# Performance work log

Hardware: AMD Instinct MI355X
Metric: run time of the kernel (lower is better)

## Reference

```python
import jax, jax.numpy as jnp
import numpy as np

# CrossAttention (DFFNet): 1x1 convs produce q,k from depth and v from rgb;
# full dense attention over hw spatial tokens: softmax(q^T k) then v @ mask^T.

def setup_inputs() -> dict:
    key = jax.random.key(0)
    ks = jax.random.split(key, 8)
    B, C, H, W = 4, 256, 64, 64
    Cqk = C // 8  # ratio=8 -> 32
    s = 0.02
    return {
        "rgb":   jax.random.normal(ks[0], (B, C, H, W), jnp.float32),
        "depth": jax.random.normal(ks[1], (B, C, H, W), jnp.float32),
        "Wq": jax.random.normal(ks[2], (Cqk, C), jnp.float32) * s,
        "bq": jax.random.normal(ks[3], (Cqk,), jnp.float32) * s,
        "Wk": jax.random.normal(ks[4], (Cqk, C), jnp.float32) * s,
        "bk": jax.random.normal(ks[5], (Cqk,), jnp.float32) * s,
        "Wv": jax.random.normal(ks[6], (C, C), jnp.float32) * s,
        "bv": jax.random.normal(ks[7], (C,), jnp.float32) * s,
    }


def reference(rgb, depth, Wq, bq, Wk, bk, Wv, bv):
    B, C, H, W = rgb.shape
    hw = H * W
    d = depth.reshape(B, C, hw)   # [B, C, hw]
    r = rgb.reshape(B, C, hw)     # [B, C, hw]
    # 1x1 convs == channel-mixing linear maps
    q = jnp.einsum('oc,bcn->bon', Wq, d) + bq[None, :, None]  # [B, Cqk, hw]
    k = jnp.einsum('oc,bcn->bon', Wk, d) + bk[None, :, None]  # [B, Cqk, hw]
    v = jnp.einsum('oc,bcn->bon', Wv, r) + bv[None, :, None]  # [B, C, hw]
    # scores: q^T k -> [B, hw, hw], softmax over last dim
    scores = jnp.einsum('bcn,bcm->bnm', q, k)
    mask = jax.nn.softmax(scores, axis=-1)
    # feat = v @ mask^T  -> [B, C, hw]
    feat = jnp.einsum('bcm,bnm->bcn', v, mask)
    return feat.reshape(B, C, H, W)
```

## Files before the change

kernel.cpp:

```cpp
#include <hip/hip_runtime.h>
#include <stdint.h>

#define L2E 1.44269504088896340736f

typedef _Float16 half8 __attribute__((ext_vector_type(8)));
typedef float floatx4 __attribute__((ext_vector_type(4)));

static __device__ __forceinline__ unsigned short f32_to_f16u(float f) {
  union { _Float16 h; unsigned short s; } cv; cv.h = (_Float16)f; return cv.s;
}

typedef __attribute__((address_space(3))) unsigned int as3_uint;
typedef __attribute__((address_space(1))) const unsigned int as1_cuint;

static __device__ __forceinline__ void async16(const void* g, void* l) {
  __builtin_amdgcn_global_load_lds((as1_cuint*)g, (as3_uint*)l, 16, 0, 0);
}

__global__ __launch_bounds__(256) void proj_kernel(
    const float* __restrict__ rgb,
    const float* __restrict__ depth,
    const float* __restrict__ Wq, const float* __restrict__ bq,
    const float* __restrict__ Wk, const float* __restrict__ bk,
    const float* __restrict__ Wv, const float* __restrict__ bv,
    unsigned short* __restrict__ qT,
    unsigned short* __restrict__ kT,
    unsigned short* __restrict__ v)
{
  __shared__ __align__(16) unsigned short sW[64 * 256];

  const int n0 = blockIdx.x * 64;
  const int b  = blockIdx.y;
  const int z  = blockIdx.z;
  const int t  = threadIdx.x;
  const int w  = t >> 6;
  const int lane = t & 63;
  const int l15 = lane & 15;
  const int q4  = lane >> 4;

  const float* X = (z == 0) ? depth : rgb;
  const float* xb = X + (size_t)b * 256 * 4096;
  const int n_row = n0 + 16 * w + l15;
  const int colbase = (z == 0) ? 0 : (z - 1) * 64;

#pragma unroll
  for (int it = 0; it < 8; it++) {
    int L = it * 256 + t;
    int og = L >> 5;
    int phys = L & 31;
    int ci = phys ^ (og & 7);
    const float* wr;
    if (z == 0) wr = (og < 32) ? (Wq + (size_t)og * 256) : (Wk + (size_t)(og - 32) * 256);
    else        wr = Wv + (size_t)(colbase + og) * 256;
    float4 w0 = *(const float4*)(wr + ci * 8);
    float4 w1 = *(const float4*)(wr + ci * 8 + 4);
    half8 h;
    h[0] = (_Float16)w0.x; h[1] = (_Float16)w0.y; h[2] = (_Float16)w0.z; h[3] = (_Float16)w0.w;
    h[4] = (_Float16)w1.x; h[5] = (_Float16)w1.y; h[6] = (_Float16)w1.z; h[7] = (_Float16)w1.w;
    *(half8*)&sW[(size_t)L * 8] = h;
  }

  float bias[4];
#pragma unroll
  for (int ct = 0; ct < 4; ct++) {
    int og = ct * 16 + l15;
    if (z == 0) bias[ct] = (og < 32) ? bq[og] : bk[og - 32];
    else        bias[ct] = bv[colbase + og];
  }
  __syncthreads();

  floatx4 acc[4];
#pragma unroll
  for (int i = 0; i < 4; i++) acc[i] = (floatx4){0.f, 0.f, 0.f, 0.f};

#pragma unroll
  for (int ks = 0; ks < 8; ks++) {
    const int c0 = ks * 32;
    half8 a;
#pragma unroll
    for (int j = 0; j < 8; j++) {
      int c = c0 + q4 * 8 + j;
      a[j] = (_Float16)xb[(size_t)c * 4096 + n_row];
    }
    const int ci = ks * 4 + q4;
#pragma unroll
    for (int ct = 0; ct < 4; ct++) {
      int og = ct * 16 + l15;
      half8 bf = *(const half8*)&sW[og * 256 + ((ci ^ (og & 7)) * 8)];
      acc[ct] = __builtin_amdgcn_mfma_f32_16x16x32_f16(a, bf, acc[ct], 0, 0, 0);
    }
  }

  __syncthreads();

  if (z == 0) {
#pragma unroll
    for (int ct = 0; ct < 4; ct++) {
      int og = ct * 16 + l15;
#pragma unroll
      for (int r = 0; r < 4; r++) {
        int n = n0 + 16 * w + q4 * 4 + r;
        unsigned short hv = f32_to_f16u(acc[ct][r] + bias[ct]);
        if (og < 32) qT[((size_t)b * 4096 + n) * 32 + og] = hv;
        else         kT[((size_t)b * 4096 + n) * 32 + (og - 32)] = hv;
      }
    }
  } else {
    unsigned short* tile = sW;
#pragma unroll
    for (int ct = 0; ct < 4; ct++) {
#pragma unroll
      for (int r = 0; r < 4; r++) {
        int co_l = ct * 16 + l15;
        int nl = 16 * w + q4 * 4 + r;
        tile[co_l * 72 + nl] = f32_to_f16u(acc[ct][r] + bias[ct]);
      }
    }
    __syncthreads();
#pragma unroll
    for (int it = 0; it < 2; it++) {
      int co_l = it * 32 + (t >> 3);
      int ch = t & 7;
      int4 val = *(const int4*)&tile[co_l * 72 + ch * 8];
      *(int4*)&v[((size_t)b * 256 + colbase + co_l) * 4096 + n0 + ch * 8] = val;
    }
  }
}

static __device__ __forceinline__ void stage_v(
    const unsigned short* __restrict__ vB, unsigned char* sbase,
    int m0, int t, int w)
{
#pragma unroll
  for (int j = 0; j < 4; j++) {
    int lin = j * 256 + t;
    int c = lin >> 2;
    int p = lin & 3;
    int lc = p ^ ((c >> 1) & 3);
    async16(&vB[(size_t)c * 4096 + m0 + lc * 8], sbase + j * 4096 + w * 1024);
  }
}

__global__ __launch_bounds__(256, 4) void attn_kernel(
    const unsigned short* __restrict__ qT,
    const unsigned short* __restrict__ kT,
    const unsigned short* __restrict__ v,
    unsigned short* __restrict__ Op,
    float* __restrict__ lW)
{
  __shared__ __align__(16) unsigned char smem[37888];
  unsigned short* sP = (unsigned short*)(smem + 32768);

  const int n0 = blockIdx.x * 64;
  const int b  = blockIdx.y;
  const int chunk = blockIdx.z;
  const int t  = threadIdx.x;
  const int w  = t >> 6;
  const int lane = t & 63;
  const int l15 = lane & 15;
  const int q4  = lane >> 4;

  half8 aq = *(const half8*)(qT + ((size_t)b * 4096 + n0 + 16 * w + l15) * 32 + q4 * 8);

  const unsigned short* vB = v + (size_t)b * 256 * 4096;
  const unsigned short* kL = kT + (size_t)b * 4096 * 32 + (size_t)l15 * 32 + q4 * 8;
  unsigned short* sPw = sP + w * 640;

  float lsum[4] = {0.f, 0.f, 0.f, 0.f};
  floatx4 acc[16];
#pragma unroll
  for (int ct = 0; ct < 16; ct++) acc[ct] = (floatx4){0.f, 0.f, 0.f, 0.f};
  const floatx4 zf = (floatx4){0.f, 0.f, 0.f, 0.f};

  const int mbase = chunk * 1024;

  stage_v(vB, smem, mbase, t, w);
  half8 kc0 = *(const half8*)(kL + (size_t)mbase * 32);
  half8 kc1 = *(const half8*)(kL + (size_t)(mbase + 16) * 32);

  int bufoff = 0;
  for (int it = 0; it < 32; ++it) {
    const int m0 = mbase + it * 32;
    half8 kn0 = kc0, kn1 = kc1;
    if (it < 31) {
      stage_v(vB, smem + (bufoff ^ 16384), m0 + 32, t, w);
      kn0 = *(const half8*)(kL + (size_t)(m0 + 32) * 32);
      kn1 = *(const half8*)(kL + (size_t)(m0 + 48) * 32);
      asm volatile("s_waitcnt vmcnt(6)" ::: "memory");
    } else {
      asm volatile("s_waitcnt vmcnt(0)" ::: "memory");
    }

    floatx4 s0 = __builtin_amdgcn_mfma_f32_16x16x32_f16(aq, kc0, zf, 0, 0, 0);
    floatx4 s1 = __builtin_amdgcn_mfma_f32_16x16x32_f16(aq, kc1, zf, 0, 0, 0);

    float p0[4], p1[4];
#pragma unroll
    for (int r = 0; r < 4; r++) {
      p0[r] = exp2f(s0[r] * L2E);
      p1[r] = exp2f(s1[r] * L2E);
      lsum[r] += p0[r] + p1[r];
    }
#pragma unroll
    for (int r = 0; r < 4; r++) {
      int row = q4 * 4 + r;
      sPw[row * 40 + l15]      = f32_to_f16u(p0[r]);
      sPw[row * 40 + 16 + l15] = f32_to_f16u(p1[r]);
    }
    asm volatile("s_waitcnt lgkmcnt(0)" ::: "memory");
    half8 ap = *(const half8*)&sPw[l15 * 40 + q4 * 8];

    __builtin_amdgcn_s_barrier();
    asm volatile("s_waitcnt lgkmcnt(0)" ::: "memory");

    const unsigned short* sVb = (const unsigned short*)(smem + bufoff);
#pragma unroll
    for (int ct = 0; ct < 16; ct++) {
      int co = ct * 16 + l15;
      half8 bv8 = *(const half8*)&sVb[co * 32 + ((q4 ^ ((co >> 1) & 3)) * 8)];
      acc[ct] = __builtin_amdgcn_mfma_f32_16x16x32_f16(ap, bv8, acc[ct], 0, 0, 0);
    }
    asm volatile("s_waitcnt lgkmcnt(0)" ::: "memory");
    __builtin_amdgcn_s_barrier();

    kc0 = kn0; kc1 = kn1;
    bufoff ^= 16384;
  }

#pragma unroll
  for (int off = 1; off < 16; off <<= 1) {
#pragma unroll
    for (int r = 0; r < 4; r++) lsum[r] += __shfl_xor(lsum[r], off);
  }
  if (l15 == 0) {
#pragma unroll
    for (int r = 0; r < 4; r++)
      lW[((size_t)chunk * 4 + b) * 4096 + n0 + 16 * w + q4 * 4 + r] = lsum[r];
  }

  unsigned short* sO = (unsigned short*)smem;
#pragma unroll
  for (int pass = 0; pass < 2; pass++) {
    __syncthreads();
#pragma unroll
    for (int cl = 0; cl < 8; cl++) {
      int ct = pass * 8 + cl;
      int co_l = cl * 16 + l15;
#pragma unroll
      for (int r = 0; r < 4; r++) {
        int nl = 16 * w + q4 * 4 + r;
        sO[co_l * 72 + nl] = f32_to_f16u(acc[ct][r]);
      }
    }
    __syncthreads();
#pragma unroll
    for (int s = 0; s < 4; s++) {
      int co_l = s * 32 + (t >> 3);
      int ch = t & 7;
      int4 val = *(const int4*)&sO[co_l * 72 + ch * 8];
      *(int4*)&Op[(((size_t)chunk * 4 + b) * 256 + pass * 128 + co_l) * 4096 + n0 + ch * 8] = val;
    }
  }
}

__global__ __launch_bounds__(256) void combine_kernel(
    const unsigned short* __restrict__ Op,
    const float* __restrict__ lW,
    float* __restrict__ out)
{
  const int t = threadIdx.x;
  const int b = blockIdx.y;
  const size_t n8 = (size_t)blockIdx.x * 2048 + (size_t)t * 8;
  const int co0 = blockIdx.z * 8;

  float sum[8] = {0.f, 0.f, 0.f, 0.f, 0.f, 0.f, 0.f, 0.f};
#pragma unroll
  for (int ch = 0; ch < 4; ch++) {
    const float* lp = lW + ((size_t)ch * 4 + b) * 4096 + n8;
    float4 a0 = *(const float4*)lp;
    float4 a1 = *(const float4*)(lp + 4);
    sum[0] += a0.x; sum[1] += a0.y; sum[2] += a0.z; sum[3] += a0.w;
    sum[4] += a1.x; sum[5] += a1.y; sum[6] += a1.z; sum[7] += a1.w;
  }
  float rl[8];
#pragma unroll
  for (int i = 0; i < 8; i++) rl[i] = 1.0f / sum[i];

#pragma unroll
  for (int cc = 0; cc < 8; cc++) {
    int co = co0 + cc;
    float o[8] = {0.f, 0.f, 0.f, 0.f, 0.f, 0.f, 0.f, 0.f};
#pragma unroll
    for (int ch = 0; ch < 4; ch++) {
      half8 hv = *(const half8*)&Op[(((size_t)ch * 4 + b) * 256 + co) * 4096 + n8];
#pragma unroll
      for (int i = 0; i < 8; i++) o[i] += (float)hv[i];
    }
    float* op = out + ((size_t)b * 256 + co) * 4096 + n8;
    float4 r0, r1;
    r0.x = o[0] * rl[0]; r0.y = o[1] * rl[1]; r0.z = o[2] * rl[2]; r0.w = o[3] * rl[3];
    r1.x = o[4] * rl[4]; r1.y = o[5] * rl[5]; r1.z = o[6] * rl[6]; r1.w = o[7] * rl[7];
    *(float4*)op = r0;
    *(float4*)(op + 4) = r1;
  }
}

extern "C" void kernel_launch(void* const* d_in, const int* in_sizes, int n_in,
                              void* d_out, int out_size, void* d_ws, size_t ws_size,
                              hipStream_t stream) {
  const float* rgb   = (const float*)d_in[0];
  const float* depth = (const float*)d_in[1];
  const float* Wq    = (const float*)d_in[2];
  const float* bq    = (const float*)d_in[3];
  const float* Wk    = (const float*)d_in[4];
  const float* bk    = (const float*)d_in[5];
  const float* Wv    = (const float*)d_in[6];
  const float* bv    = (const float*)d_in[7];
  float* out = (float*)d_out;

  unsigned short* qT = (unsigned short*)d_ws;
  unsigned short* kT = qT + (size_t)4 * 4096 * 32;
  unsigned short* vW = kT + (size_t)4 * 4096 * 32;
  unsigned short* Op = vW + (size_t)4 * 256 * 4096;
  float* lW = (float*)(Op + (size_t)4 * 4 * 256 * 4096);

  dim3 pg(64, 4, 5);
  proj_kernel<<<pg, 256, 0, stream>>>(rgb, depth, Wq, bq, Wk, bk, Wv, bv, qT, kT, vW);
  dim3 ag(64, 4, 4);
  attn_kernel<<<ag, 256, 0, stream>>>(qT, kT, vW, Op, lW);
  dim3 cg(2, 4, 32);
  combine_kernel<<<cg, 256, 0, stream>>>(Op, lW, out);
}
```

Measured before the change: 168.1 us.

## Reuse loaded activations across V channel groups and retile attention PV per wave

The projection kernel now loads each thread's input activation fragment into registers once and loops over two 64-channel output groups of V per block. This halves the grid's z extent and avoids re-reading the rgb tensor for each group. In the attention kernel, each wave now owns a 64-channel slice of V and reads all four waves' P tiles from shared memory. Each V fragment is then reused across four MFMAs instead of every wave loading all 256 V channels, which cuts LDS read traffic but needs the whole shared P buffer visible after the barrier.

```diff
diff --git a/kernel.cpp b/kernel.cpp
--- a/kernel.cpp
+++ b/kernel.cpp
@@ -41,88 +41,96 @@
   const float* X = (z == 0) ? depth : rgb;
   const float* xb = X + (size_t)b * 256 * 4096;
   const int n_row = n0 + 16 * w + l15;
-  const int colbase = (z == 0) ? 0 : (z - 1) * 64;
-
-#pragma unroll
-  for (int it = 0; it < 8; it++) {
-    int L = it * 256 + t;
-    int og = L >> 5;
-    int phys = L & 31;
-    int ci = phys ^ (og & 7);
-    const float* wr;
-    if (z == 0) wr = (og < 32) ? (Wq + (size_t)og * 256) : (Wk + (size_t)(og - 32) * 256);
-    else        wr = Wv + (size_t)(colbase + og) * 256;
-    float4 w0 = *(const float4*)(wr + ci * 8);
-    float4 w1 = *(const float4*)(wr + ci * 8 + 4);
-    half8 h;
-    h[0] = (_Float16)w0.x; h[1] = (_Float16)w0.y; h[2] = (_Float16)w0.z; h[3] = (_Float16)w0.w;
-    h[4] = (_Float16)w1.x; h[5] = (_Float16)w1.y; h[6] = (_Float16)w1.z; h[7] = (_Float16)w1.w;
-    *(half8*)&sW[(size_t)L * 8] = h;
-  }
-
-  float bias[4];
-#pragma unroll
-  for (int ct = 0; ct < 4; ct++) {
-    int og = ct * 16 + l15;
-    if (z == 0) bias[ct] = (og < 32) ? bq[og] : bk[og - 32];
-    else        bias[ct] = bv[colbase + og];
-  }
-  __syncthreads();
-
-  floatx4 acc[4];
-#pragma unroll
-  for (int i = 0; i < 4; i++) acc[i] = (floatx4){0.f, 0.f, 0.f, 0.f};
-
+
+  half8 a8[8];
 #pragma unroll
   for (int ks = 0; ks < 8; ks++) {
-    const int c0 = ks * 32;
-    half8 a;
 #pragma unroll
     for (int j = 0; j < 8; j++) {
-      int c = c0 + q4 * 8 + j;
-      a[j] = (_Float16)xb[(size_t)c * 4096 + n_row];
-    }
-    const int ci = ks * 4 + q4;
+      int c = ks * 32 + q4 * 8 + j;
+      a8[ks][j] = (_Float16)xb[(size_t)c * 4096 + n_row];
+    }
+  }
+
+  const int nq = (z == 0) ? 1 : 2;
+  for (int qd = 0; qd < nq; qd++) {
+    const int colbase = (z == 0) ? 0 : (z - 1) * 128 + qd * 64;
+    __syncthreads();
+
+#pragma unroll
+    for (int it = 0; it < 8; it++) {
+      int L = it * 256 + t;
+      int og = L >> 5;
+      int phys = L & 31;
+      int ci = phys ^ (og & 7);
+      const float* wr;
+      if (z == 0) wr = (og < 32) ? (Wq + (size_t)og * 256) : (Wk + (size_t)(og - 32) * 256);
+      else        wr = Wv + (size_t)(colbase + og) * 256;
+      float4 w0 = *(const float4*)(wr + ci * 8);
+      float4 w1 = *(const float4*)(wr + ci * 8 + 4);
+      half8 h;
+      h[0] = (_Float16)w0.x; h[1] = (_Float16)w0.y; h[2] = (_Float16)w0.z; h[3] = (_Float16)w0.w;
+      h[4] = (_Float16)w1.x; h[5] = (_Float16)w1.y; h[6] = (_Float16)w1.z; h[7] = (_Float16)w1.w;
+      *(half8*)&sW[(size_t)L * 8] = h;
+    }
+
+    float bias[4];
 #pragma unroll
     for (int ct = 0; ct < 4; ct++) {
       int og = ct * 16 + l15;
-      half8 bf = *(const half8*)&sW[og * 256 + ((ci ^ (og & 7)) * 8)];
-      acc[ct] = __builtin_amdgcn_mfma_f32_16x16x32_f16(a, bf, acc[ct], 0, 0, 0);
-    }
-  }
-
-  __syncthreads();
-
-  if (z == 0) {
-#pragma unroll
-    for (int ct = 0; ct < 4; ct++) {
-      int og = ct * 16 + l15;
-#pragma unroll
-      for (int r = 0; r < 4; r++) {
-        int n = n0 + 16 * w + q4 * 4 + r;
-        unsigned short hv = f32_to_f16u(acc[ct][r] + bias[ct]);
-        if (og < 32) qT[((size_t)b * 4096 + n) * 32 + og] = hv;
-        else         kT[((size_t)b * 4096 + n) * 32 + (og - 32)] = hv;
-      }
-    }
-  } else {
-    unsigned short* tile = sW;
-#pragma unroll
-    for (int ct = 0; ct < 4; ct++) {
-#pragma unroll
-      for (int r = 0; r < 4; r++) {
-        int co_l = ct * 16 + l15;
-        int nl = 16 * w + q4 * 4 + r;
-        tile[co_l * 72 + nl] = f32_to_f16u(acc[ct][r] + bias[ct]);
-      }
-    }
-    __syncthreads();
-#pragma unroll
-    for (int it = 0; it < 2; it++) {
-      int co_l = it * 32 + (t >> 3);
-      int ch = t & 7;
-      int4 val = *(const int4*)&tile[co_l * 72 + ch * 8];
-      *(int4*)&v[((size_t)b * 256 + colbase + co_l) * 4096 + n0 + ch * 8] = val;
+      if (z == 0) bias[ct] = (og < 32) ? bq[og] : bk[og - 32];
+      else        bias[ct] = bv[colbase + og];
+    }
+    __syncthreads();
+
+    floatx4 acc[4];
+#pragma unroll
+    for (int i = 0; i < 4; i++) acc[i] = (floatx4){0.f, 0.f, 0.f, 0.f};
+
+#pragma unroll
+    for (int ks = 0; ks < 8; ks++) {
+      const int ci = ks * 4 + q4;
+#pragma unroll
+      for (int ct = 0; ct < 4; ct++) {
+        int og = ct * 16 + l15;
+        half8 bf = *(const half8*)&sW[og * 256 + ((ci ^ (og & 7)) * 8)];
+        acc[ct] = __builtin_amdgcn_mfma_f32_16x16x32_f16(a8[ks], bf, acc[ct], 0, 0, 0);
+      }
+    }
+
+    __syncthreads();
+
+    if (z == 0) {
+#pragma unroll
+      for (int ct = 0; ct < 4; ct++) {
+        int og = ct * 16 + l15;
+#pragma unroll
+        for (int r = 0; r < 4; r++) {
+          int n = n0 + 16 * w + q4 * 4 + r;
+          unsigned short hv = f32_to_f16u(acc[ct][r] + bias[ct]);
+          if (og < 32) qT[((size_t)b * 4096 + n) * 32 + og] = hv;
+          else         kT[((size_t)b * 4096 + n) * 32 + (og - 32)] = hv;
+        }
+      }
+    } else {
+      unsigned short* tile = sW;
+#pragma unroll
+      for (int ct = 0; ct < 4; ct++) {
+#pragma unroll
+        for (int r = 0; r < 4; r++) {
+          int co_l = ct * 16 + l15;
+          int nl = 16 * w + q4 * 4 + r;
+          tile[co_l * 72 + nl] = f32_to_f16u(acc[ct][r] + bias[ct]);
+        }
+      }
+      __syncthreads();
+#pragma unroll
+      for (int it = 0; it < 2; it++) {
+        int co_l = it * 32 + (t >> 3);
+        int ch = t & 7;
+        int4 val = *(const int4*)&tile[co_l * 72 + ch * 8];
+        *(int4*)&v[((size_t)b * 256 + colbase + co_l) * 4096 + n0 + ch * 8] = val;
+      }
     }
   }
 }
@@ -208,17 +216,23 @@
       sPw[row * 40 + 16 + l15] = f32_to_f16u(p1[r]);
     }
     asm volatile("s_waitcnt lgkmcnt(0)" ::: "memory");
-    half8 ap = *(const half8*)&sPw[l15 * 40 + q4 * 8];
 
     __builtin_amdgcn_s_barrier();
     asm volatile("s_waitcnt lgkmcnt(0)" ::: "memory");
 
+    half8 ap[4];
+#pragma unroll
+    for (int nt = 0; nt < 4; nt++)
+      ap[nt] = *(const half8*)&sP[nt * 640 + l15 * 40 + q4 * 8];
+
     const unsigned short* sVb = (const unsigned short*)(smem + bufoff);
 #pragma unroll
-    for (int ct = 0; ct < 16; ct++) {
-      int co = ct * 16 + l15;
+    for (int ct = 0; ct < 4; ct++) {
+      int co = w * 64 + ct * 16 + l15;
       half8 bv8 = *(const half8*)&sVb[co * 32 + ((q4 ^ ((co >> 1) & 3)) * 8)];
-      acc[ct] = __builtin_amdgcn_mfma_f32_16x16x32_f16(ap, bv8, acc[ct], 0, 0, 0);
+#pragma unroll
+      for (int nt = 0; nt < 4; nt++)
+        acc[ct * 4 + nt] = __builtin_amdgcn_mfma_f32_16x16x32_f16(ap[nt], bv8, acc[ct * 4 + nt], 0, 0, 0);
     }
     asm volatile("s_waitcnt lgkmcnt(0)" ::: "memory");
     __builtin_amdgcn_s_barrier();
@@ -242,14 +256,18 @@
 #pragma unroll
   for (int pass = 0; pass < 2; pass++) {
     __syncthreads();
-#pragma unroll
-    for (int cl = 0; cl < 8; cl++) {
-      int ct = pass * 8 + cl;
-      int co_l = cl * 16 + l15;
-#pragma unroll
-      for (int r = 0; r < 4; r++) {
-        int nl = 16 * w + q4 * 4 + r;
-        sO[co_l * 72 + nl] = f32_to_f16u(acc[ct][r]);
+    if ((w >> 1) == pass) {
+#pragma unroll
+      for (int ct = 0; ct < 4; ct++) {
+        int co_l = (w & 1) * 64 + ct * 16 + l15;
+#pragma unroll
+        for (int nt = 0; nt < 4; nt++) {
+#pragma unroll
+          for (int r = 0; r < 4; r++) {
+            int nl = nt * 16 + q4 * 4 + r;
+            sO[co_l * 72 + nl] = f32_to_f16u(acc[ct * 4 + nt][r]);
+          }
+        }
       }
     }
     __syncthreads();
@@ -324,7 +342,7 @@
   unsigned short* Op = vW + (size_t)4 * 256 * 4096;
   float* lW = (float*)(Op + (size_t)4 * 4 * 256 * 4096);
 
-  dim3 pg(64, 4, 5);
+  dim3 pg(64, 4, 3);
   proj_kernel<<<pg, 256, 0, stream>>>(rgb, depth, Wq, bq, Wk, bk, Wv, bv, qT, kT, vW);
   dim3 ag(64, 4, 4);
   attn_kernel<<<ag, 256, 0, stream>>>(qT, kT, vW, Op, lW);
```

Measured after the change: 163.5 us. 1.03x faster.
